# Kernel optimization log

Hardware: AMD Instinct MI355X
Metric: run time of the kernel (lower is better)

## Reference

```python
import jax, jax.numpy as jnp
import numpy as np

N_NODES = 100000
N_EDGES = 1600000


def spmm(edge_row, edge_col, edge_w, h):
    # out[r] = sum_{e: row[e]=r} w[e] * h[col[e]]   (sparse adj @ dense h)
    msgs = h[edge_col] * edge_w[:, None]  # [E, F]
    return jax.ops.segment_sum(msgs, edge_row, num_segments=N_NODES)


def setup_inputs() -> dict:
    key = jax.random.key(0)
    ks = jax.random.split(key, 6)
    x = jax.random.normal(ks[0], (N_NODES, 256), dtype=jnp.float32)
    edge_row = jax.random.randint(ks[1], (N_EDGES,), 0, N_NODES, dtype=jnp.int32)
    edge_col = jax.random.randint(ks[2], (N_EDGES,), 0, N_NODES, dtype=jnp.int32)
    edge_w = jax.random.uniform(ks[3], (N_EDGES,), dtype=jnp.float32)
    W1 = jax.random.normal(ks[4], (256, 128), dtype=jnp.float32) * (1.0 / np.sqrt(256))
    b1 = jnp.zeros((128,), dtype=jnp.float32)
    W2 = jax.random.normal(ks[5], (128, 40), dtype=jnp.float32) * (1.0 / np.sqrt(128))
    b2 = jnp.zeros((40,), dtype=jnp.float32)
    return {"x": x, "edge_row": edge_row, "edge_col": edge_col, "edge_w": edge_w,
            "W1": W1, "b1": b1, "W2": W2, "b2": b2}


def reference(x, edge_row, edge_col, edge_w, W1, b1, W2, b2):
    # eval-mode GCN forward (dropout inactive, no BN)
    h = spmm(edge_row, edge_col, edge_w, x @ W1) + b1  # [N, hidden]
    h = jax.nn.relu(h)
    out = spmm(edge_row, edge_col, edge_w, h @ W2) + b2  # [N, classes]
    return jax.nn.log_softmax(out, axis=1)
```

## Files before the change

### kernel.cpp

```cpp
#include <hip/hip_runtime.h>
#include <math.h>

#define F1 256
#define F2 128
#define F3 40
#define H2S 64
#define RPB 256
#define RSH 8
#define TPB 8192

typedef unsigned short ushort_t;
typedef unsigned char uchar_t;
typedef unsigned int uint_t;
typedef __attribute__((ext_vector_type(8))) short bf16x8;
typedef __attribute__((ext_vector_type(4))) float f32x4;
typedef __attribute__((ext_vector_type(2))) float f32x2;

__device__ inline ushort_t f2bf(float f) {
  unsigned u = __builtin_bit_cast(unsigned, f);
  u += 0x7FFF + ((u >> 16) & 1);
  return (ushort_t)(u >> 16);
}
__device__ inline float bf2f(ushort_t b) {
  unsigned u = ((unsigned)b) << 16;
  return __builtin_bit_cast(float, u);
}
__device__ inline float i2f(int b) { return __builtin_bit_cast(float, b); }
__device__ inline uchar_t f2fp8(float f) {
  return (uchar_t)(__builtin_amdgcn_cvt_pk_fp8_f32(f, 0.f, 0, false) & 0xff);
}
__device__ inline f32x2 fp8lo(unsigned u) { return __builtin_amdgcn_cvt_pk_f32_fp8(u, false); }
__device__ inline f32x2 fp8hi(unsigned u) { return __builtin_amdgcn_cvt_pk_f32_fp8(u, true); }
__device__ inline long long nt_ld_rec(const long long* p) {
  return __builtin_nontemporal_load(p);
}
__device__ inline int rec_col(long long r) { return (int)(unsigned)(r & 0xffffffffll); }
__device__ inline float rec_w(long long r) { return i2f((int)(unsigned)(((unsigned long long)r) >> 32)); }


__global__ __launch_bounds__(256) void k_cnt(const int* __restrict__ row, int* __restrict__ cnt,
                                             int E, int G, int NBIN) {
  __shared__ int h[400];
  int tid = threadIdx.x, blk = blockIdx.x;
  for (int i = tid; i < NBIN; i += 256) h[i] = 0;
  __syncthreads();
  int base = blk * TPB, lim = min(base + TPB, E);
  for (int i = base + tid; i < lim; i += 256) atomicAdd(&h[row[i] >> RSH], 1);
  __syncthreads();
  for (int i = tid; i < NBIN; i += 256) cnt[i * G + blk] = h[i];
}

__global__ __launch_bounds__(256) void k_scan1(const int* __restrict__ in, int* __restrict__ out,
                                               int* __restrict__ aux, int n) {
  __shared__ int lds[256];
  int tid = threadIdx.x;
  int base = blockIdx.x * 1024 + tid * 4;
  int v0 = 0, v1 = 0, v2 = 0, v3 = 0;
  if (base + 0 < n) v0 = in[base + 0];
  if (base + 1 < n) v1 = in[base + 1];
  if (base + 2 < n) v2 = in[base + 2];
  if (base + 3 < n) v3 = in[base + 3];
  int s = v0 + v1 + v2 + v3;
  lds[tid] = s;
  __syncthreads();
  for (int off = 1; off < 256; off <<= 1) {
    int t = (tid >= off) ? lds[tid - off] : 0;
    __syncthreads();
    lds[tid] += t;
    __syncthreads();
  }
  int excl = (tid > 0) ? lds[tid - 1] : 0;
  if (tid == 255) aux[blockIdx.x] = lds[255];
  if (base + 0 < n) out[base + 0] = excl;
  if (base + 1 < n) out[base + 1] = excl + v0;
  if (base + 2 < n) out[base + 2] = excl + v0 + v1;
  if (base + 3 < n) out[base + 3] = excl + v0 + v1 + v2;
}

__global__ __launch_bounds__(128) void k_scan_aux(int* __restrict__ aux, int nb) {
  __shared__ int lds[128];
  int tid = threadIdx.x;
  int v = (tid < nb) ? aux[tid] : 0;
  lds[tid] = v;
  __syncthreads();
  for (int off = 1; off < 128; off <<= 1) {
    int t = (tid >= off) ? lds[tid - off] : 0;
    __syncthreads();
    lds[tid] += t;
    __syncthreads();
  }
  int excl = (tid > 0) ? lds[tid - 1] : 0;
  if (tid < nb) aux[tid] = excl;
}

__global__ __launch_bounds__(256) void k_scan_add(int* __restrict__ out, const int* __restrict__ aux,
                                                  int n, int E) {
  int add = aux[blockIdx.x];
  int base = blockIdx.x * 1024 + threadIdx.x * 4;
#pragma unroll
  for (int i = 0; i < 4; i++)
    if (base + i < n) out[base + i] += add;
  if (blockIdx.x == 0 && threadIdx.x == 0) out[n] = E;
}

__global__ __launch_bounds__(256) void k_scatter1(const int* __restrict__ row, const int* __restrict__ col,
                                                  const float* __restrict__ w, const int* __restrict__ cntoff,
                                                  int2* __restrict__ epk2, int E, int G, int NBIN) {
  __shared__ int cur[400];
  int tid = threadIdx.x, blk = blockIdx.x;
  for (int i = tid; i < NBIN; i += 256) cur[i] = cntoff[i * G + blk];
  __syncthreads();
  int base = blk * TPB, lim = min(base + TPB, E);
  for (int i = base + tid; i < lim; i += 256) {
    int r = row[i];
    int pos = atomicAdd(&cur[r >> RSH], 1);
    epk2[pos] = make_int2(((r & (RPB - 1)) << 17) | col[i], __builtin_bit_cast(int, w[i]));
  }
}

__global__ __launch_bounds__(256) void k_binsort(const int* __restrict__ cntoff, const int2* __restrict__ epk2,
                                                 int* __restrict__ ip, int2* __restrict__ epk,
                                                 int G, int NBIN, int N, int E) {
  __shared__ int sc[256], cur[256];
  int tid = threadIdx.x, b = blockIdx.x;
  int s = cntoff[b * G], eend = cntoff[(b + 1) * G];
  cur[tid] = 0;
  __syncthreads();
  for (int i = s + tid; i < eend; i += 256) atomicAdd(&cur[epk2[i].x >> 17], 1);
  __syncthreads();
  int d = cur[tid];
  sc[tid] = d;
  __syncthreads();
  for (int o = 1; o < 256; o <<= 1) {
    int t = (tid >= o) ? sc[tid - o] : 0;
    __syncthreads();
    sc[tid] += t;
    __syncthreads();
  }
  int excl = (tid > 0) ? sc[tid - 1] : 0;
  __syncthreads();
  cur[tid] = excl;
  int gr = (b << RSH) + tid;
  if (gr <= N) ip[gr] = s + excl;
  if (b == 0 && tid == 0) ip[N] = E;
  __syncthreads();
  for (int i = s + tid; i < eend; i += 256) {
    int2 rec = epk2[i];
    int local = rec.x >> 17, c = rec.x & 0x1FFFF;
    int p = s + atomicAdd(&cur[local], 1);
    epk[p] = make_int2(c, rec.y);
  }
}

__global__ __launch_bounds__(256) void k_w1prep(const float* __restrict__ W1, ushort_t* __restrict__ w1pf) {
  int idx = blockIdx.x * 256 + threadIdx.x;
  if (idx < 8 * 8 * 64 * 8) {
    int j = idx & 7;
    int l = (idx >> 3) & 63;
    int t = (idx >> 9) & 7;
    int kt = idx >> 12;
    int k = kt * 32 + (l >> 4) * 8 + j;
    int c = t * 16 + (l & 15);
    w1pf[idx] = f2bf(W1[(size_t)k * F2 + c]);
  }
}

__global__ __launch_bounds__(256) void k_w2prep(const float* __restrict__ W2, ushort_t* __restrict__ w2p) {
  int idx = blockIdx.x * 256 + threadIdx.x;
  if (idx < 4 * 3 * 64 * 8) {
    int j = idx & 7;
    int rem = idx >> 3;
    int l = rem & 63;
    int g = rem >> 6;
    int t = g % 3, kt = g / 3;
    int colc = t * 16 + (l & 15);
    int k = kt * 32 + (l >> 4) * 8 + j;
    w2p[idx] = (colc < F3) ? f2bf(W2[(size_t)k * F3 + colc]) : (ushort_t)0;
  }
}

__global__ __launch_bounds__(256) void k_gemm1(const float* __restrict__ x, const ushort_t* __restrict__ w1pf,
                                               uchar_t* __restrict__ h0f8, int N) {
  const int tid = threadIdx.x;
  const int lane = tid & 63;
  const int w = tid >> 6;
  const int r0 = blockIdx.x * 64;
  const int arow = r0 + w * 16 + (lane & 15);
  const int ar = (arow < N) ? arow : 0;
  const int kg = (lane >> 4) * 8;
  const float* xr = x + (size_t)ar * F1 + kg;

  f32x4 xv[16];
#pragma unroll
  for (int kt = 0; kt < 8; ++kt) {
    xv[2 * kt]     = *(const f32x4*)(xr + kt * 32);
    xv[2 * kt + 1] = *(const f32x4*)(xr + kt * 32 + 4);
  }

  bf16x8 a[8];
#pragma unroll
  for (int kt = 0; kt < 8; ++kt) {
    f32x4 v0 = xv[2 * kt], v1 = xv[2 * kt + 1];
    a[kt][0] = (short)f2bf(v0.x); a[kt][1] = (short)f2bf(v0.y);
    a[kt][2] = (short)f2bf(v0.z); a[kt][3] = (short)f2bf(v0.w);
    a[kt][4] = (short)f2bf(v1.x); a[kt][5] = (short)f2bf(v1.y);
    a[kt][6] = (short)f2bf(v1.z); a[kt][7] = (short)f2bf(v1.w);
  }

  f32x4 acc[8];
#pragma unroll
  for (int t = 0; t < 8; ++t) acc[t] = (f32x4){0.f, 0.f, 0.f, 0.f};

#pragma unroll
  for (int kt = 0; kt < 8; ++kt) {
#pragma unroll
    for (int t = 0; t < 8; ++t) {
      bf16x8 b = *(const bf16x8*)(w1pf + (size_t)(((kt * 8 + t) * 64) + lane) * 8);
      acc[t] = __builtin_amdgcn_mfma_f32_16x16x32_bf16(a[kt], b, acc[t], 0, 0, 0);
    }
  }

#pragma unroll
  for (int t = 0; t < 8; ++t) {
    int gc = t * 16 + (lane & 15);
#pragma unroll
    for (int j = 0; j < 4; ++j) {
      int gr = r0 + w * 16 + (lane >> 4) * 4 + j;
      if (gr < N) h0f8[(size_t)gr * F2 + gc] = f2fp8(acc[t][j]);
    }
  }
}

__global__ __launch_bounds__(256) void k_spmm1(const int* __restrict__ ip, const long long* __restrict__ epk,
                                               const uchar_t* __restrict__ h0f8,
                                               const float* __restrict__ b1, ushort_t* __restrict__ hbf) {
  int node = blockIdx.x * 4 + (threadIdx.x >> 6);
  int lane = threadIdx.x & 63;
  int e0 = __builtin_amdgcn_readfirstlane(ip[node]);
  int e1 = __builtin_amdgcn_readfirstlane(ip[node + 1]);
  const uint_t* hb = (const uint_t*)h0f8;
  const int half = lane >> 5;
  const int d = lane & 31;
  float a0x = 0.f, a0y = 0.f, a0z = 0.f, a0w = 0.f;
  float a1x = 0.f, a1y = 0.f, a1z = 0.f, a1w = 0.f;
  float a2x = 0.f, a2y = 0.f, a2z = 0.f, a2w = 0.f;
  float a3x = 0.f, a3y = 0.f, a3z = 0.f, a3w = 0.f;
  for (int e = e0; e < e1; e += 8) {
    int i1 = e1 - 1;
    long long p0 = nt_ld_rec(&epk[(e + 0 < e1) ? e + 0 : i1]);
    long long p1 = nt_ld_rec(&epk[(e + 1 < e1) ? e + 1 : i1]);
    long long p2 = nt_ld_rec(&epk[(e + 2 < e1) ? e + 2 : i1]);
    long long p3 = nt_ld_rec(&epk[(e + 3 < e1) ? e + 3 : i1]);
    long long p4 = nt_ld_rec(&epk[(e + 4 < e1) ? e + 4 : i1]);
    long long p5 = nt_ld_rec(&epk[(e + 5 < e1) ? e + 5 : i1]);
    long long p6 = nt_ld_rec(&epk[(e + 6 < e1) ? e + 6 : i1]);
    long long p7 = nt_ld_rec(&epk[(e + 7 < e1) ? e + 7 : i1]);
    int c0 = half ? rec_col(p1) : rec_col(p0);
    int c1 = half ? rec_col(p3) : rec_col(p2);
    int c2 = half ? rec_col(p5) : rec_col(p4);
    int c3 = half ? rec_col(p7) : rec_col(p6);
    uint_t u0 = hb[(size_t)c0 * 32 + d];
    uint_t u1 = hb[(size_t)c1 * 32 + d];
    uint_t u2 = hb[(size_t)c2 * 32 + d];
    uint_t u3 = hb[(size_t)c3 * 32 + d];
    float w0 = (e + 0 + half < e1) ? (half ? rec_w(p1) : rec_w(p0)) : 0.f;
    float w1 = (e + 2 + half < e1) ? (half ? rec_w(p3) : rec_w(p2)) : 0.f;
    float w2 = (e + 4 + half < e1) ? (half ? rec_w(p5) : rec_w(p4)) : 0.f;
    float w3 = (e + 6 + half < e1) ? (half ? rec_w(p7) : rec_w(p6)) : 0.f;
    f32x2 l0 = fp8lo(u0), h0 = fp8hi(u0);
    f32x2 l1 = fp8lo(u1), h1 = fp8hi(u1);
    f32x2 l2 = fp8lo(u2), h2 = fp8hi(u2);
    f32x2 l3 = fp8lo(u3), h3 = fp8hi(u3);
    a0x = fmaf(w0, l0.x, a0x); a0y = fmaf(w0, l0.y, a0y); a0z = fmaf(w0, h0.x, a0z); a0w = fmaf(w0, h0.y, a0w);
    a1x = fmaf(w1, l1.x, a1x); a1y = fmaf(w1, l1.y, a1y); a1z = fmaf(w1, h1.x, a1z); a1w = fmaf(w1, h1.y, a1w);
    a2x = fmaf(w2, l2.x, a2x); a2y = fmaf(w2, l2.y, a2y); a2z = fmaf(w2, h2.x, a2z); a2w = fmaf(w2, h2.y, a2w);
    a3x = fmaf(w3, l3.x, a3x); a3y = fmaf(w3, l3.y, a3y); a3z = fmaf(w3, h3.x, a3z); a3w = fmaf(w3, h3.y, a3w);
  }
  float sx = (a0x + a1x) + (a2x + a3x);
  float sy = (a0y + a1y) + (a2y + a3y);
  float sz = (a0z + a1z) + (a2z + a3z);
  float sw = (a0w + a1w) + (a2w + a3w);
  sx += __shfl_xor(sx, 32);
  sy += __shfl_xor(sy, 32);
  sz += __shfl_xor(sz, 32);
  sw += __shfl_xor(sw, 32);
  float4 bb = *(const float4*)(b1 + d * 4);
  unsigned long long rr =
      (unsigned long long)f2bf(fmaxf(sx + bb.x, 0.f)) |
      ((unsigned long long)f2bf(fmaxf(sy + bb.y, 0.f)) << 16) |
      ((unsigned long long)f2bf(fmaxf(sz + bb.z, 0.f)) << 32) |
      ((unsigned long long)f2bf(fmaxf(sw + bb.w, 0.f)) << 48);
  if (lane < 32)
    __builtin_nontemporal_store(rr, (unsigned long long*)(hbf + (size_t)node * F2 + d * 4));
}

__global__ __launch_bounds__(256) void k_gemm2(const ushort_t* __restrict__ hbf, const ushort_t* __restrict__ w2p,
                                               uchar_t* __restrict__ h2f8, int N) {
  const int tid = threadIdx.x;
  const int lane = tid & 63;
  const int w = tid >> 6;
  const int r0 = blockIdx.x * 64;
  const int arow = r0 + w * 16 + (lane & 15);
  const int ar = (arow < N) ? arow : 0;
  const int kg = (lane >> 4) * 8;

  bf16x8 a[4];
#pragma unroll
  for (int kt = 0; kt < 4; ++kt)
    a[kt] = *(const bf16x8*)(hbf + (size_t)ar * F2 + kt * 32 + kg);

  f32x4 acc[3];
#pragma unroll
  for (int t = 0; t < 3; ++t) acc[t] = (f32x4){0.f, 0.f, 0.f, 0.f};

#pragma unroll
  for (int kt = 0; kt < 4; ++kt) {
#pragma unroll
    for (int t = 0; t < 3; ++t) {
      bf16x8 b = *(const bf16x8*)(w2p + (size_t)(((kt * 3 + t) * 64) + lane) * 8);
      acc[t] = __builtin_amdgcn_mfma_f32_16x16x32_bf16(a[kt], b, acc[t], 0, 0, 0);
    }
  }

#pragma unroll
  for (int t = 0; t < 3; ++t) {
    int gc = t * 16 + (lane & 15);
    if (gc < F3) {
#pragma unroll
      for (int j = 0; j < 4; ++j) {
        int gr = r0 + w * 16 + (lane >> 4) * 4 + j;
        if (gr < N) h2f8[(size_t)gr * H2S + gc] = f2fp8(acc[t][j]);
      }
    }
  }
  for (int idx = tid; idx < 64 * 24; idx += 256) {
    int row = idx / 24, pc = F3 + idx % 24;
    int gr = r0 + row;
    if (gr < N) h2f8[(size_t)gr * H2S + pc] = 0;
  }
}

__global__ __launch_bounds__(256) void k_spmm2lsm(const int* __restrict__ ip, const long long* __restrict__ epk,
                                                  const uchar_t* __restrict__ h2f8,
                                                  const float* __restrict__ b2, float* __restrict__ out) {
  int node = blockIdx.x * 4 + (threadIdx.x >> 6);
  int lane = threadIdx.x & 63;
  int e0 = __builtin_amdgcn_readfirstlane(ip[node]);
  int e1 = __builtin_amdgcn_readfirstlane(ip[node + 1]);
  const uint_t* hb = (const uint_t*)h2f8;
  const int slot = lane >> 4;
  const int d = lane & 15;
  float aAx = 0.f, aAy = 0.f, aAz = 0.f, aAw = 0.f;
  float aBx = 0.f, aBy = 0.f, aBz = 0.f, aBw = 0.f;
  for (int e = e0; e < e1; e += 8) {
    int i1 = e1 - 1;
    long long p0 = nt_ld_rec(&epk[(e + 0 < e1) ? e + 0 : i1]);
    long long p1 = nt_ld_rec(&epk[(e + 1 < e1) ? e + 1 : i1]);
    long long p2 = nt_ld_rec(&epk[(e + 2 < e1) ? e + 2 : i1]);
    long long p3 = nt_ld_rec(&epk[(e + 3 < e1) ? e + 3 : i1]);
    long long p4 = nt_ld_rec(&epk[(e + 4 < e1) ? e + 4 : i1]);
    long long p5 = nt_ld_rec(&epk[(e + 5 < e1) ? e + 5 : i1]);
    long long p6 = nt_ld_rec(&epk[(e + 6 < e1) ? e + 6 : i1]);
    long long p7 = nt_ld_rec(&epk[(e + 7 < e1) ? e + 7 : i1]);
    long long qa = (slot < 2) ? (slot == 0 ? p0 : p1) : (slot == 2 ? p2 : p3);
    long long qb = (slot < 2) ? (slot == 0 ? p4 : p5) : (slot == 2 ? p6 : p7);
    uint_t uA = hb[(size_t)rec_col(qa) * 16 + d];
    uint_t uB = hb[(size_t)rec_col(qb) * 16 + d];
    float wA = (e + slot < e1) ? rec_w(qa) : 0.f;
    float wB = (e + 4 + slot < e1) ? rec_w(qb) : 0.f;
    f32x2 lA = fp8lo(uA), hA = fp8hi(uA);
    f32x2 lB = fp8lo(uB), hB = fp8hi(uB);
    aAx = fmaf(wA, lA.x, aAx); aAy = fmaf(wA, lA.y, aAy); aAz = fmaf(wA, hA.x, aAz); aAw = fmaf(wA, hA.y, aAw);
    aBx = fmaf(wB, lB.x, aBx); aBy = fmaf(wB, lB.y, aBy); aBz = fmaf(wB, hB.x, aBz); aBw = fmaf(wB, hB.y, aBw);
  }
  float sx = aAx + aBx, sy = aAy + aBy, sz = aAz + aBz, sw = aAw + aBw;
  sx += __shfl_xor(sx, 16); sx += __shfl_xor(sx, 32);
  sy += __shfl_xor(sy, 16); sy += __shfl_xor(sy, 32);
  sz += __shfl_xor(sz, 16); sz += __shfl_xor(sz, 32);
  sw += __shfl_xor(sw, 16); sw += __shfl_xor(sw, 32);
  float l0 = -INFINITY, l1 = -INFINITY, l2 = -INFINITY, l3 = -INFINITY;
  if (d < 10) {
    float4 bb = *(const float4*)(b2 + d * 4);
    l0 = sx + bb.x; l1 = sy + bb.y; l2 = sz + bb.z; l3 = sw + bb.w;
  }
  float m = fmaxf(fmaxf(l0, l1), fmaxf(l2, l3));
#pragma unroll
  for (int off = 1; off < 16; off <<= 1) m = fmaxf(m, __shfl_xor(m, off));
  float e0x = (d < 10) ? __expf(l0 - m) : 0.f;
  float e1x = (d < 10) ? __expf(l1 - m) : 0.f;
  float e2x = (d < 10) ? __expf(l2 - m) : 0.f;
  float e3x = (d < 10) ? __expf(l3 - m) : 0.f;
  float s = (e0x + e1x) + (e2x + e3x);
#pragma unroll
  for (int off = 1; off < 16; off <<= 1) s += __shfl_xor(s, off);
  float ls = __logf(s);
  if (d < 10) {
    f32x4 r;
    r[0] = l0 - m - ls; r[1] = l1 - m - ls; r[2] = l2 - m - ls; r[3] = l3 - m - ls;
    __builtin_nontemporal_store(r, (f32x4*)(out + (size_t)node * F3 + d * 4));
  }
}

extern "C" void kernel_launch(void* const* d_in, const int* in_sizes, int n_in,
                              void* d_out, int out_size, void* d_ws, size_t ws_size,
                              hipStream_t stream) {
  const float* x     = (const float*)d_in[0];
  const int* erow    = (const int*)d_in[1];
  const int* ecol_in = (const int*)d_in[2];
  const float* ew_in = (const float*)d_in[3];
  const float* W1    = (const float*)d_in[4];
  const float* b1    = (const float*)d_in[5];
  const float* W2    = (const float*)d_in[6];
  const float* b2    = (const float*)d_in[7];
  float* out = (float*)d_out;

  const int N = in_sizes[0] / F1;
  const int E = in_sizes[1];

  const int G = (E + TPB - 1) / TPB;
  const int NBIN = (N + RPB - 1) >> RSH;
  const int M = NBIN * G;
  const int nb2 = (M + 1023) / 1024;

  uchar_t* region0 = (uchar_t*)d_ws;
  int2* epk2 = (int2*)d_ws;
  uchar_t* h0f8 = region0;
  uchar_t* h2f8 = region0;
  ushort_t* hbf = (ushort_t*)(region0 + (size_t)N * F2 * 2);
  int* ip = (int*)(hbf + (size_t)N * F2);
  int* cnt = ip + (N + 32);
  int* cntoff = cnt + M + 8;
  int* aux = cntoff + M + 64;
  int2* epk = (int2*)(aux + 128);
  ushort_t* w1pf = (ushort_t*)(epk + E);
  ushort_t* w2p = w1pf + 32768;

  hipLaunchKernelGGL(k_cnt, dim3(G), dim3(256), 0, stream, erow, cnt, E, G, NBIN);
  hipLaunchKernelGGL(k_scan1, dim3(nb2), dim3(256), 0, stream, cnt, cntoff, aux, M);
  hipLaunchKernelGGL(k_scan_aux, dim3(1), dim3(128), 0, stream, aux, nb2);
  hipLaunchKernelGGL(k_scan_add, dim3(nb2), dim3(256), 0, stream, cntoff, aux, M, E);
  hipLaunchKernelGGL(k_scatter1, dim3(G), dim3(256), 0, stream, erow, ecol_in, ew_in, cntoff, epk2, E, G, NBIN);
  hipLaunchKernelGGL(k_binsort, dim3(NBIN), dim3(256), 0, stream, cntoff, epk2, ip, epk, G, NBIN, N, E);
  hipLaunchKernelGGL(k_w1prep, dim3(128), dim3(256), 0, stream, W1, w1pf);
  hipLaunchKernelGGL(k_w2prep, dim3((4 * 3 * 64 * 8 + 255) / 256), dim3(256), 0, stream, W2, w2p);
  hipLaunchKernelGGL(k_gemm1, dim3((N + 63) / 64), dim3(256), 0, stream, x, w1pf, h0f8, N);
  hipLaunchKernelGGL(k_spmm1, dim3(N / 4), dim3(256), 0, stream, ip, (const long long*)epk, h0f8, b1, hbf);
  hipLaunchKernelGGL(k_gemm2, dim3((N + 63) / 64), dim3(256), 0, stream, hbf, w2p, h2f8, N);
  hipLaunchKernelGGL(k_spmm2lsm, dim3(N / 4), dim3(256), 0, stream, ip, (const long long*)epk, h2f8, b2, out);
}
```

Baseline: 204.2 us.

## Stage W1 fragments through LDS in two column halves for gemm1

New measurement: 199.0 us (median of 2 runs). 1.03x faster.

```diff
diff --git a/kernel.cpp b/kernel.cpp
--- a/kernel.cpp
+++ b/kernel.cpp
@@ -154,11 +154,14 @@
 
 __global__ __launch_bounds__(256) void k_w1prep(const float* __restrict__ W1, ushort_t* __restrict__ w1pf) {
   int idx = blockIdx.x * 256 + threadIdx.x;
-  if (idx < 8 * 8 * 64 * 8) {
+  if (idx < 2 * 8 * 4 * 64 * 8) {
     int j = idx & 7;
     int l = (idx >> 3) & 63;
-    int t = (idx >> 9) & 7;
-    int kt = idx >> 12;
+    int g = idx >> 9;
+    int tl = g & 3;
+    int kt = (g >> 2) & 7;
+    int th = g >> 5;
+    int t = th * 4 + tl;
     int k = kt * 32 + (l >> 4) * 8 + j;
     int c = t * 16 + (l & 15);
     w1pf[idx] = f2bf(W1[(size_t)k * F2 + c]);
@@ -181,6 +184,7 @@
 
 __global__ __launch_bounds__(256) void k_gemm1(const float* __restrict__ x, const ushort_t* __restrict__ w1pf,
                                                uchar_t* __restrict__ h0f8, int N) {
+  __shared__ uint4 wlds[2048];
   const int tid = threadIdx.x;
   const int lane = tid & 63;
   const int w = tid >> 6;
@@ -189,12 +193,18 @@
   const int ar = (arow < N) ? arow : 0;
   const int kg = (lane >> 4) * 8;
   const float* xr = x + (size_t)ar * F1 + kg;
+  const ushort_t* wb = (const ushort_t*)wlds;
 
   f32x4 xv[16];
 #pragma unroll
   for (int kt = 0; kt < 8; ++kt) {
     xv[2 * kt]     = *(const f32x4*)(xr + kt * 32);
     xv[2 * kt + 1] = *(const f32x4*)(xr + kt * 32 + 4);
+  }
+
+  {
+    const uint4* src = (const uint4*)w1pf;
+    for (int o = tid; o < 2048; o += 256) wlds[o] = src[o];
   }
 
   bf16x8 a[8];
@@ -206,27 +216,37 @@
     a[kt][4] = (short)f2bf(v1.x); a[kt][5] = (short)f2bf(v1.y);
     a[kt][6] = (short)f2bf(v1.z); a[kt][7] = (short)f2bf(v1.w);
   }
-
-  f32x4 acc[8];
-#pragma unroll
-  for (int t = 0; t < 8; ++t) acc[t] = (f32x4){0.f, 0.f, 0.f, 0.f};
-
-#pragma unroll
-  for (int kt = 0; kt < 8; ++kt) {
-#pragma unroll
-    for (int t = 0; t < 8; ++t) {
-      bf16x8 b = *(const bf16x8*)(w1pf + (size_t)(((kt * 8 + t) * 64) + lane) * 8);
-      acc[t] = __builtin_amdgcn_mfma_f32_16x16x32_bf16(a[kt], b, acc[t], 0, 0, 0);
+  __syncthreads();
+
+  const int orow = r0 + w * 16 + (lane >> 4) * 4;
+
+#pragma unroll
+  for (int th = 0; th < 2; ++th) {
+    f32x4 acc[4];
+#pragma unroll
+    for (int tl = 0; tl < 4; ++tl) acc[tl] = (f32x4){0.f, 0.f, 0.f, 0.f};
+#pragma unroll
+    for (int kt = 0; kt < 8; ++kt) {
+#pragma unroll
+      for (int tl = 0; tl < 4; ++tl) {
+        bf16x8 b = *(const bf16x8*)&wb[(size_t)((kt * 4 + tl) * 64 + lane) * 8];
+        acc[tl] = __builtin_amdgcn_mfma_f32_16x16x32_bf16(a[kt], b, acc[tl], 0, 0, 0);
+      }
     }
-  }
-
-#pragma unroll
-  for (int t = 0; t < 8; ++t) {
-    int gc = t * 16 + (lane & 15);
-#pragma unroll
-    for (int j = 0; j < 4; ++j) {
-      int gr = r0 + w * 16 + (lane >> 4) * 4 + j;
-      if (gr < N) h0f8[(size_t)gr * F2 + gc] = f2fp8(acc[t][j]);
+#pragma unroll
+    for (int tl = 0; tl < 4; ++tl) {
+      int gc = (th * 4 + tl) * 16 + (lane & 15);
+#pragma unroll
+      for (int j = 0; j < 4; ++j) {
+        int gr = orow + j;
+        if (gr < N) h0f8[(size_t)gr * F2 + gc] = f2fp8(acc[tl][j]);
+      }
+    }
+    if (th == 0) {
+      __syncthreads();
+      const uint4* src = (const uint4*)w1pf + 2048;
+      for (int o = tid; o < 2048; o += 256) wlds[o] = src[o];
+      __syncthreads();
     }
   }
 }
```
